# Performance work log

Hardware: AMD Instinct MI355X
Metric: run time of the kernel (lower is better)

## Reference

```python
import jax, jax.numpy as jnp
import numpy as np

B, T, C, H = 2, 2048, 1024, 16
D = C // H  # head dim = 64


def setup_inputs() -> dict:
    key = jax.random.key(0)
    k1, k2, k3 = jax.random.split(key, 3)
    x = jax.random.normal(k1, (B, T, C), dtype=jnp.float32)
    w_attn = jax.random.normal(k2, (C, 3 * C), dtype=jnp.float32) * (1.0 / np.sqrt(C))
    b_attn = jnp.zeros((3 * C,), dtype=jnp.float32)
    w_proj = jax.random.normal(k3, (C, C), dtype=jnp.float32) * (1.0 / np.sqrt(C))
    b_proj = jnp.zeros((C,), dtype=jnp.float32)
    return {"x": x, "w_attn": w_attn, "b_attn": b_attn, "w_proj": w_proj, "b_proj": b_proj}


def reference(x, w_attn, b_attn, w_proj, b_proj):
    Bx, Tx, Cx = x.shape
    qkv = x @ w_attn + b_attn  # [B, T, 3C]
    q, k, v = jnp.split(qkv, 3, axis=-1)
    # [B, H, T, D]
    q = q.reshape(Bx, Tx, H, D).swapaxes(1, 2)
    k = k.reshape(Bx, Tx, H, D).swapaxes(1, 2)
    v = v.reshape(Bx, Tx, H, D).swapaxes(1, 2)
    scale = 1.0 / jnp.sqrt(jnp.float32(D))
    att = jnp.einsum('bhqd,bhkd->bhqk', q, k) * scale  # [B, H, T, T]
    causal = jnp.tril(jnp.ones((Tx, Tx), dtype=bool))
    att = jnp.where(causal[None, None], att, -jnp.inf)
    att = jax.nn.softmax(att, axis=-1)
    y = jnp.einsum('bhqk,bhkd->bhqd', att, v)  # [B, H, T, D]
    y = y.swapaxes(1, 2).reshape(Bx, Tx, Cx)
    return y @ w_proj + b_proj
```

## Files before the change

### kernel.cpp

```cpp
#include <hip/hip_runtime.h>
#include <hip/hip_bf16.h>


typedef __attribute__((ext_vector_type(8))) short short8x;
typedef __attribute__((ext_vector_type(4))) float float4x;
typedef __attribute__((ext_vector_type(4))) unsigned short ushort4x;
typedef __attribute__((ext_vector_type(2))) unsigned int uint2x;

#define MFMA_BF16 __builtin_amdgcn_mfma_f32_16x16x32_bf16

typedef const __attribute__((address_space(1))) void gvoid_t;
typedef __attribute__((address_space(3))) void lvoid_t;
#define GLOAD_LDS16(g, l) __builtin_amdgcn_global_load_lds((gvoid_t*)(g), (lvoid_t*)(l), 16, 0, 0)

__device__ __forceinline__ unsigned short f2b(float f) {
    unsigned int u = __float_as_uint(f);
    u = (u + 0x7FFFu + ((u >> 16) & 1u)) >> 16;
    return (unsigned short)u;
}
__device__ __forceinline__ unsigned int pk2(float a, float b) {
    return __builtin_amdgcn_perm(__float_as_uint(b) + 0x8000u,
                                 __float_as_uint(a) + 0x8000u, 0x07060302u);
}
__device__ __forceinline__ unsigned int pk2t(float a, float b) {
    return __builtin_amdgcn_perm(__float_as_uint(b),
                                 __float_as_uint(a), 0x07060302u);
}

__device__ __forceinline__ void stage32(const unsigned short* g, size_t rs,
                                        short* ldst, int w0, int lane) {
    const int r8 = lane >> 3;
    const int sc = ((lane & 7) ^ r8) * 8;
#pragma unroll
    for (int q = 0; q < 4; q++) {
        GLOAD_LDS16(g + (size_t)(w0 + q * 8 + r8) * rs + sc,
                    ldst + (w0 + q * 8) * 64);
    }
}

__global__ __launch_bounds__(256) void prep(const float* __restrict__ x,
                                            unsigned short* __restrict__ xb,
                                            const float* __restrict__ wa,
                                            unsigned short* __restrict__ waT,
                                            const float* __restrict__ wp,
                                            unsigned short* __restrict__ wpT) {
    __shared__ float tile[32][33];
    const int blk = blockIdx.x;
    if (blk < 4096) {
        int i = blk * 256 + threadIdx.x;
        float4 v = ((const float4*)x)[i];
        ushort4x o = { f2b(v.x), f2b(v.y), f2b(v.z), f2b(v.w) };
        ((ushort4x*)xb)[i] = o;
        return;
    }
    int idx = blk - 4096;
    int bx = idx & 127;
    int by = idx >> 7;
    const float* in;
    unsigned short* outp;
    int cols;
    if (bx < 96) { in = wa; outp = waT; cols = 3072; }
    else         { in = wp; outp = wpT; cols = 1024; bx -= 96; }
    const int tx = threadIdx.x & 31, ty = threadIdx.x >> 5;
    const int cbase = bx * 32, rbase = by * 32;
    int c = cbase + tx;
    for (int j = 0; j < 32; j += 8)
        tile[ty + j][tx] = in[(size_t)(rbase + ty + j) * cols + c];
    __syncthreads();
    int rr = rbase + tx;
    for (int j = 0; j < 32; j += 8) {
        int cc = cbase + ty + j;
        outp[(size_t)cc * 1024 + rr] = f2b(tile[tx][ty + j]);
    }
}

template <bool SWAP>
__device__ __forceinline__ void qkv_mainloop(const unsigned short* Ag,
                                             const unsigned short* Bg,
                                             short* lA, short* lB,
                                             float4x (&acc)[4][4],
                                             int wave, int lane, int wr, int wc,
                                             int quad, int l16, int sw) {
    const int K = 1024;
    for (int kk = 0; kk < K; kk += 64) {
        stage32(Ag + kk, K, lA, wave * 32, lane);
        stage32(Bg + kk, K, lB, wave * 32, lane);
        __syncthreads();

#pragma unroll
        for (int kk2 = 0; kk2 < 2; kk2++) {
            short8x a[4], b[4];
#pragma unroll
            for (int i = 0; i < 4; i++)
                a[i] = *(const short8x*)&lA[(wr * 64 + i * 16 + l16) * 64 +
                                            ((kk2 * 4 + quad) ^ sw) * 8];
#pragma unroll
            for (int j = 0; j < 4; j++)
                b[j] = *(const short8x*)&lB[(wc * 64 + j * 16 + l16) * 64 +
                                            ((kk2 * 4 + quad) ^ sw) * 8];
#pragma unroll
            for (int i = 0; i < 4; i++)
#pragma unroll
                for (int j = 0; j < 4; j++)
                    acc[i][j] = SWAP ? MFMA_BF16(b[j], a[i], acc[i][j], 0, 0, 0)
                                     : MFMA_BF16(a[i], b[j], acc[i][j], 0, 0, 0);
        }
        __syncthreads();
    }
}

__global__ __launch_bounds__(256, 4) void gemm_qkv(const unsigned short* __restrict__ A,
                                                   const unsigned short* __restrict__ BT,
                                                   const float* __restrict__ bias,
                                                   unsigned short* __restrict__ QK,
                                                   unsigned short* __restrict__ VTg) {
    __shared__ union {
        struct { short A[128 * 64]; short B[128 * 64]; } s;
        short vt[4][64 * 80];
    } lds;

    const int K = 1024;
    const int lane = threadIdx.x & 63;
    const int wave = threadIdx.x >> 6;
    const int quad = lane >> 4;
    const int l16  = lane & 15;
    const int sw   = l16 & 7;

    const int rblk = blockIdx.y * 128;
    const int cblk = blockIdx.x * 128;
    const int wr = wave >> 1, wc = wave & 1;
    const bool qk = (blockIdx.x < 16);

    float4x acc[4][4] = {};

    const unsigned short* Ag = A  + (size_t)rblk * K;
    const unsigned short* Bg = BT + (size_t)cblk * K;

    if (qk) qkv_mainloop<true >(Ag, Bg, lds.s.A, lds.s.B, acc, wave, lane, wr, wc, quad, l16, sw);
    else    qkv_mainloop<false>(Ag, Bg, lds.s.A, lds.s.B, acc, wave, lane, wr, wc, quad, l16, sw);

    const int rbase = rblk + wr * 64;
    const int cbase = cblk + wc * 64;

    if (qk) {
        const float sc = (blockIdx.x < 8) ? 0.18033688f : 1.0f;
#pragma unroll
        for (int i = 0; i < 4; i++) {
            const int r = rbase + i * 16 + l16;
#pragma unroll
            for (int j = 0; j < 4; j++) {
                const int c = cbase + j * 16 + quad * 4;
                float4 bv = *(const float4*)&bias[c];
                uint2x p = { pk2((acc[i][j][0] + bv.x) * sc, (acc[i][j][1] + bv.y) * sc),
                             pk2((acc[i][j][2] + bv.z) * sc, (acc[i][j][3] + bv.w) * sc) };
                *(uint2x*)&QK[(size_t)r * 2048 + c] = p;
            }
        }
    } else {
#pragma unroll
        for (int i = 0; i < 4; i++) {
#pragma unroll
            for (int j = 0; j < 4; j++) {
                int c = cbase + j * 16 + l16;
                float bv = bias[c];
                uint2x p = { pk2(acc[i][j][0] + bv, acc[i][j][1] + bv),
                             pk2(acc[i][j][2] + bv, acc[i][j][3] + bv) };
                *(uint2x*)&lds.vt[wave][(j * 16 + l16) * 80 + i * 16 + quad * 4] = p;
            }
        }
        const int h   = (cbase - 2048) >> 6;
        const int hb  = (rbase >> 11) * 16 + h;
        const int tb0 = rbase & 2047;
#pragma unroll
        for (int p = 0; p < 8; p++) {
            int dd   = p * 8 + (lane >> 3);
            int toff = (lane & 7) * 8;
            short8x vv = *(const short8x*)&lds.vt[wave][dd * 80 + toff];
            *(short8x*)&VTg[((size_t)(hb * 64 + dd)) * 2048 + tb0 + toff] = vv;
        }
    }
}

__global__ __launch_bounds__(256) void gemm_proj(const unsigned short* __restrict__ A,
                                                 const unsigned short* __restrict__ BT,
                                                 const float* __restrict__ bias,
                                                 float* __restrict__ out) {
    __shared__ struct { short A[2][64 * 64]; short B[2][128 * 64]; } lds;

    const int K = 1024, N = 1024;
    const int lane = threadIdx.x & 63;
    const int wave = threadIdx.x >> 6;
    const int quad = lane >> 4;
    const int l16  = lane & 15;
    const int sw   = l16 & 7;

    const int rblk = blockIdx.y * 64;
    const int cblk = blockIdx.x * 128;

    float4x acc[4][2] = {};

    const unsigned short* Ag = A  + (size_t)rblk * K;
    const unsigned short* Bg = BT + (size_t)cblk * K;

    for (int kk = 0; kk < K; kk += 128) {
#pragma unroll
        for (int t = 0; t < 3; t++) {
            const int u = wave * 3 + t;
            if (u < 4) {
                stage32(Ag + kk + (u >> 1) * 64, K, lds.A[u >> 1], (u & 1) * 32, lane);
            } else {
                const int v = u - 4;
                stage32(Bg + kk + (v >> 2) * 64, K, lds.B[v >> 2], (v & 3) * 32, lane);
            }
        }
        __syncthreads();

#pragma unroll
        for (int kp = 0; kp < 2; kp++) {
#pragma unroll
            for (int kk2 = 0; kk2 < 2; kk2++) {
                short8x b[2];
#pragma unroll
                for (int j = 0; j < 2; j++)
                    b[j] = *(const short8x*)&lds.B[kp][(wave * 32 + j * 16 + l16) * 64 +
                                                       ((kk2 * 4 + quad) ^ sw) * 8];
#pragma unroll
                for (int i = 0; i < 4; i++) {
                    short8x a = *(const short8x*)&lds.A[kp][(i * 16 + l16) * 64 +
                                                            ((kk2 * 4 + quad) ^ sw) * 8];
#pragma unroll
                    for (int j = 0; j < 2; j++)
                        acc[i][j] = MFMA_BF16(a, b[j], acc[i][j], 0, 0, 0);
                }
            }
        }
        __syncthreads();
    }

#pragma unroll
    for (int j = 0; j < 2; j++) {
        const int c = cblk + wave * 32 + j * 16 + l16;
        const float bv = bias[c];
#pragma unroll
        for (int i = 0; i < 4; i++) {
#pragma unroll
            for (int reg = 0; reg < 4; reg++) {
                int r = rblk + i * 16 + quad * 4 + reg;
                out[(size_t)r * N + c] = acc[i][j][reg] + bv;
            }
        }
    }
}

__global__ __launch_bounds__(256) void attn_kernel(const unsigned short* __restrict__ QK,
                                                   const unsigned short* __restrict__ VT,
                                                   unsigned short* __restrict__ Y) {
    __shared__ __attribute__((aligned(16))) short Kl[2][64 * 64];
    __shared__ __attribute__((aligned(16))) short Vl[2][64 * 64];
    __shared__ __attribute__((aligned(16))) short Pl[4][2048];

    const int tid  = threadIdx.x;
    const int lane = tid & 63;
    const int wave = tid >> 6;
    const int quad = lane >> 4;
    const int l16  = lane & 15;
    const int sw   = l16 & 7;

    const int bid = blockIdx.x;
    const int qb  = 31 - (bid >> 5);
    const int bh  = bid & 31;
    const int b = bh >> 4, h = bh & 15;

    const unsigned short* Qp = QK + ((size_t)b * 2048) * 2048 + h * 64;
    const unsigned short* Kp = Qp + 1024;
    const unsigned short* Vp = VT + (size_t)bh * 64 * 2048;

    const int qbase = qb * 64 + wave * 16;
    const int ntb   = qb + 1;

    short8x aq[2];
#pragma unroll
    for (int kk = 0; kk < 2; kk++)
        aq[kk] = *(const short8x*)(Qp + (size_t)(qbase + l16) * 2048 + kk * 32 + quad * 8);

    const short ONE = (short)0x3F80;
    const short8x ones = { ONE, ONE, ONE, ONE, ONE, ONE, ONE, ONE };

    if (wave < 2) stage32(Kp, 2048, Kl[0], wave * 32, lane);
    else          stage32(Vp, 2048, Vl[0], (wave - 2) * 32, lane);
    __syncthreads();

    float4x lacc = {};
    float4x O[4] = {};

    for (int it = 0; it < ntb; it++) {
        const int kb = it * 64;
        const short* Kc = Kl[it & 1];
        const short* Vc = Vl[it & 1];

        if (it + 1 < ntb) {
            const int kb2 = kb + 64;
            if (wave < 2) stage32(Kp + (size_t)kb2 * 2048, 2048, Kl[(it + 1) & 1], wave * 32, lane);
            else          stage32(Vp + kb2, 2048, Vl[(it + 1) & 1], (wave - 2) * 32, lane);
        }

        float4x S[4];
#pragma unroll
        for (int t = 0; t < 4; t++) {
            short8x kf0 = *(const short8x*)&Kc[(t * 16 + l16) * 64 + ((quad) ^ sw) * 8];
            short8x kf1 = *(const short8x*)&Kc[(t * 16 + l16) * 64 + ((4 + quad) ^ sw) * 8];
            S[t] = (float4x){0.f, 0.f, 0.f, 0.f};
            S[t] = MFMA_BF16(kf0, aq[0], S[t], 0, 0, 0);
            S[t] = MFMA_BF16(kf1, aq[1], S[t], 0, 0, 0);
        }

        if (kb + 64 > qbase) {
            int q = qbase + l16;
#pragma unroll
            for (int t = 0; t < 4; t++)
#pragma unroll
                for (int reg = 0; reg < 4; reg++)
                    if (kb + t * 16 + quad * 4 + reg > q) S[t][reg] = -1e38f;
        }

#pragma unroll
        for (int t = 0; t < 4; t++) {
            float e0 = __builtin_amdgcn_exp2f(S[t][0]);
            float e1 = __builtin_amdgcn_exp2f(S[t][1]);
            float e2 = __builtin_amdgcn_exp2f(S[t][2]);
            float e3 = __builtin_amdgcn_exp2f(S[t][3]);
            uint2x p = { pk2t(e0, e1), pk2t(e2, e3) };
            *(uint2x*)&Pl[wave][l16 * 64 + ((2 * t + (quad >> 1)) ^ sw) * 8 + (quad & 1) * 4] = p;
        }

#pragma unroll
        for (int kc = 0; kc < 2; kc++) {
            short8x bp = *(const short8x*)&Pl[wave][l16 * 64 + ((4 * kc + quad) ^ sw) * 8];
            lacc = MFMA_BF16(ones, bp, lacc, 0, 0, 0);
#pragma unroll
            for (int dt = 0; dt < 4; dt++) {
                short8x vf = *(const short8x*)&Vc[(dt * 16 + l16) * 64 + ((kc * 4 + quad) ^ sw) * 8];
                O[dt] = MFMA_BF16(vf, bp, O[dt], 0, 0, 0);
            }
        }
        __syncthreads();
    }

    float rl = 1.0f / lacc[0];
#pragma unroll
    for (int dt = 0; dt < 4; dt++) {
        uint2x o = { pk2(O[dt][0] * rl, O[dt][1] * rl),
                     pk2(O[dt][2] * rl, O[dt][3] * rl) };
        *(uint2x*)&Pl[wave][l16 * 64 + ((2 * dt + (quad >> 1)) ^ sw) * 8 + (quad & 1) * 4] = o;
    }
    const int t = qbase + l16;
#pragma unroll
    for (int cc = 0; cc < 2; cc++) {
        short8x row = *(const short8x*)&Pl[wave][l16 * 64 + ((2 * quad + cc) ^ sw) * 8];
        *(short8x*)&Y[((size_t)(b * 2048 + t)) * 1024 + h * 64 + (2 * quad + cc) * 8] = row;
    }
}

extern "C" void kernel_launch(void* const* d_in, const int* in_sizes, int n_in,
                              void* d_out, int out_size, void* d_ws, size_t ws_size,
                              hipStream_t stream) {
    const float* x      = (const float*)d_in[0];
    const float* w_attn = (const float*)d_in[1];
    const float* b_attn = (const float*)d_in[2];
    const float* w_proj = (const float*)d_in[3];
    const float* b_proj = (const float*)d_in[4];
    float* out = (float*)d_out;

    char* ws = (char*)d_ws;
    unsigned short* xb  = (unsigned short*)(ws + (size_t)0);
    unsigned short* waT = (unsigned short*)(ws + (size_t)(8  << 20));
    unsigned short* wpT = (unsigned short*)(ws + (size_t)(14 << 20));
    unsigned short* QKb = (unsigned short*)(ws + (size_t)(16 << 20));
    unsigned short* VTb = (unsigned short*)(ws + (size_t)(32 << 20));
    unsigned short* yb  = (unsigned short*)(ws + (size_t)(40 << 20));

    prep<<<8192, 256, 0, stream>>>(x, xb, w_attn, waT, w_proj, wpT);

    gemm_qkv<<<dim3(24, 32), 256, 0, stream>>>(xb, waT, b_attn, QKb, VTb);

    attn_kernel<<<1024, 256, 0, stream>>>(QKb, VTb, yb);

    gemm_proj<<<dim3(8, 64), 256, 0, stream>>>(yb, wpT, b_proj, out);
}
```

Baseline: 163.4 us.

## Software-pipeline attention loop so QK-softmax of tile overlaps PV of previous tile

Splits the attention loop body into two parts: a QK-plus-exponent stage and a PV accumulation stage. The loop is restructured so that the PV product of tile it-1 runs before the barrier, and the QK/softmax of tile it runs after it. The P staging buffer is indexed per parity, which double-buffers it, and the next K/V stage is issued right after the barrier. The aim is to interleave exp/VALU work with MFMA work and to shorten barrier stalls. In exchange it needs twice the per-wave P LDS space and adds a prologue and an epilogue.

```diff
diff --git a/kernel.cpp b/kernel.cpp
--- a/kernel.cpp
+++ b/kernel.cpp
@@ -286,65 +286,76 @@
     const short ONE = (short)0x3F80;
     const short8x ones = { ONE, ONE, ONE, ONE, ONE, ONE, ONE, ONE };
 
+    float4x lacc = {};
+    float4x O[4] = {};
+
+    auto QKSM = [&](int t) {
+        const short* Kc = Kl[t & 1];
+        const int kb = t * 64;
+        short* Pb = &Pl[wave][(t & 1) * 1024];
+        float4x S[4];
+#pragma unroll
+        for (int tt = 0; tt < 4; tt++) {
+            short8x kf0 = *(const short8x*)&Kc[(tt * 16 + l16) * 64 + ((quad) ^ sw) * 8];
+            short8x kf1 = *(const short8x*)&Kc[(tt * 16 + l16) * 64 + ((4 + quad) ^ sw) * 8];
+            S[tt] = (float4x){0.f, 0.f, 0.f, 0.f};
+            S[tt] = MFMA_BF16(kf0, aq[0], S[tt], 0, 0, 0);
+            S[tt] = MFMA_BF16(kf1, aq[1], S[tt], 0, 0, 0);
+        }
+        if (kb + 64 > qbase) {
+            int q = qbase + l16;
+#pragma unroll
+            for (int tt = 0; tt < 4; tt++)
+#pragma unroll
+                for (int reg = 0; reg < 4; reg++)
+                    if (kb + tt * 16 + quad * 4 + reg > q) S[tt][reg] = -1e38f;
+        }
+#pragma unroll
+        for (int tt = 0; tt < 4; tt++) {
+            float e0 = __builtin_amdgcn_exp2f(S[tt][0]);
+            float e1 = __builtin_amdgcn_exp2f(S[tt][1]);
+            float e2 = __builtin_amdgcn_exp2f(S[tt][2]);
+            float e3 = __builtin_amdgcn_exp2f(S[tt][3]);
+            uint2x p = { pk2t(e0, e1), pk2t(e2, e3) };
+            *(uint2x*)&Pb[l16 * 64 + ((2 * tt + (quad >> 1)) ^ sw) * 8 + (quad & 1) * 4] = p;
+        }
+    };
+
+    auto PV = [&](int t) {
+        const short* Vc = Vl[t & 1];
+        const short* Pb = &Pl[wave][(t & 1) * 1024];
+#pragma unroll
+        for (int kc = 0; kc < 2; kc++) {
+            short8x bp = *(const short8x*)&Pb[l16 * 64 + ((4 * kc + quad) ^ sw) * 8];
+            lacc = MFMA_BF16(ones, bp, lacc, 0, 0, 0);
+#pragma unroll
+            for (int dt = 0; dt < 4; dt++) {
+                short8x vf = *(const short8x*)&Vc[(dt * 16 + l16) * 64 + ((kc * 4 + quad) ^ sw) * 8];
+                O[dt] = MFMA_BF16(vf, bp, O[dt], 0, 0, 0);
+            }
+        }
+    };
+
     if (wave < 2) stage32(Kp, 2048, Kl[0], wave * 32, lane);
     else          stage32(Vp, 2048, Vl[0], (wave - 2) * 32, lane);
     __syncthreads();
-
-    float4x lacc = {};
-    float4x O[4] = {};
-
-    for (int it = 0; it < ntb; it++) {
-        const int kb = it * 64;
-        const short* Kc = Kl[it & 1];
-        const short* Vc = Vl[it & 1];
-
+    if (ntb > 1) {
+        if (wave < 2) stage32(Kp + (size_t)64 * 2048, 2048, Kl[1], wave * 32, lane);
+        else          stage32(Vp + 64, 2048, Vl[1], (wave - 2) * 32, lane);
+    }
+    QKSM(0);
+
+    for (int it = 1; it < ntb; it++) {
+        PV(it - 1);
+        __syncthreads();
         if (it + 1 < ntb) {
-            const int kb2 = kb + 64;
+            const int kb2 = (it + 1) * 64;
             if (wave < 2) stage32(Kp + (size_t)kb2 * 2048, 2048, Kl[(it + 1) & 1], wave * 32, lane);
             else          stage32(Vp + kb2, 2048, Vl[(it + 1) & 1], (wave - 2) * 32, lane);
         }
-
-        float4x S[4];
-#pragma unroll
-        for (int t = 0; t < 4; t++) {
-            short8x kf0 = *(const short8x*)&Kc[(t * 16 + l16) * 64 + ((quad) ^ sw) * 8];
-            short8x kf1 = *(const short8x*)&Kc[(t * 16 + l16) * 64 + ((4 + quad) ^ sw) * 8];
-            S[t] = (float4x){0.f, 0.f, 0.f, 0.f};
-            S[t] = MFMA_BF16(kf0, aq[0], S[t], 0, 0, 0);
-            S[t] = MFMA_BF16(kf1, aq[1], S[t], 0, 0, 0);
-        }
-
-        if (kb + 64 > qbase) {
-            int q = qbase + l16;
-#pragma unroll
-            for (int t = 0; t < 4; t++)
-#pragma unroll
-                for (int reg = 0; reg < 4; reg++)
-                    if (kb + t * 16 + quad * 4 + reg > q) S[t][reg] = -1e38f;
-        }
-
-#pragma unroll
-        for (int t = 0; t < 4; t++) {
-            float e0 = __builtin_amdgcn_exp2f(S[t][0]);
-            float e1 = __builtin_amdgcn_exp2f(S[t][1]);
-            float e2 = __builtin_amdgcn_exp2f(S[t][2]);
-            float e3 = __builtin_amdgcn_exp2f(S[t][3]);
-            uint2x p = { pk2t(e0, e1), pk2t(e2, e3) };
-            *(uint2x*)&Pl[wave][l16 * 64 + ((2 * t + (quad >> 1)) ^ sw) * 8 + (quad & 1) * 4] = p;
-        }
-
-#pragma unroll
-        for (int kc = 0; kc < 2; kc++) {
-            short8x bp = *(const short8x*)&Pl[wave][l16 * 64 + ((4 * kc + quad) ^ sw) * 8];
-            lacc = MFMA_BF16(ones, bp, lacc, 0, 0, 0);
-#pragma unroll
-            for (int dt = 0; dt < 4; dt++) {
-                short8x vf = *(const short8x*)&Vc[(dt * 16 + l16) * 64 + ((kc * 4 + quad) ^ sw) * 8];
-                O[dt] = MFMA_BF16(vf, bp, O[dt], 0, 0, 0);
-            }
-        }
-        __syncthreads();
-    }
+        QKSM(it);
+    }
+    PV(ntb - 1);
 
     float rl = 1.0f / lacc[0];
 #pragma unroll
```

New measurement: 166.2 us. About the same (+1.7%).
